# Kernel tuning notes

Hardware: AMD Instinct MI355X
Metric: run time of the kernel (lower is better)

The kernel has to match this reference:

```python
import jax, jax.numpy as jnp
import numpy as np

B, S, D = 2, 2048, 1024
H, DK, DV = 16, 64, 64
DFF = 4096
EPS_RMS = 1e-6


def setup_inputs() -> dict:
    key = jax.random.key(0)
    ks = jax.random.split(key, 10)
    sc = 0.02
    return {
        "x": jax.random.normal(ks[0], (B, S, D), jnp.float32),
        "w_q": jax.random.normal(ks[1], (D, H * DK), jnp.float32) * sc,
        "w_k": jax.random.normal(ks[2], (D, H * DK), jnp.float32) * sc,
        "w_v": jax.random.normal(ks[3], (D, H * DV), jnp.float32) * sc,
        "w_o": jax.random.normal(ks[4], (H * DV, D), jnp.float32) * sc,
        "w_gate": jax.random.normal(ks[5], (D, DFF), jnp.float32) * sc,
        "w_up": jax.random.normal(ks[6], (D, DFF), jnp.float32) * sc,
        "w_down": jax.random.normal(ks[7], (DFF, D), jnp.float32) * sc,
        "g1": jnp.ones((D,), jnp.float32),
        "g2": jnp.ones((D,), jnp.float32),
    }


def _rmsnorm(x, g):
    var = jnp.mean(jnp.square(x), axis=-1, keepdims=True)
    return x * jax.lax.rsqrt(var + EPS_RMS) * g


def _stable_softmax(s):
    # Faithful to source: exp(x) / (sum exp(x) + 1e-9); fully-masked rows -> 0.
    e = jnp.exp(s)
    return e / (jnp.sum(e, axis=-1, keepdims=True) + 1e-9)


def reference(x, w_q, w_k, w_v, w_o, w_gate, w_up, w_down, g1, g2):
    b, s, d = x.shape
    h = _rmsnorm(x, g1)
    q = (h @ w_q).reshape(b, s, H, DK).transpose(0, 2, 1, 3)  # [B,H,S,DK]
    k = (h @ w_k).reshape(b, s, H, DK).transpose(0, 2, 1, 3)
    v = (h @ w_v).reshape(b, s, H, DV).transpose(0, 2, 1, 3)
    scores = jnp.einsum("bhqd,bhkd->bhqk", q, k) / jnp.sqrt(jnp.asarray(DK, x.dtype))
    # triu with diagonal=0: self and future positions are masked
    mask = jnp.triu(jnp.ones((s, s), bool))
    scores = jnp.where(mask, -jnp.inf, scores)
    attn = _stable_softmax(scores)  # [B,H,S,S]
    av = jnp.einsum("bhqk,bhkd->bhqd", attn, v)
    av = av.transpose(0, 2, 1, 3).reshape(b, s, H * DV)
    x = x + av @ w_o  # residual 1
    h2 = _rmsnorm(x, g2)
    hidden = jax.nn.silu(h2 @ w_gate) * (h2 @ w_up)
    return x + hidden @ w_down  # residual 2
```

## Files before the change

kernel.cpp:

```cpp
#include <hip/hip_runtime.h>
#include <cstdint>
#include <cstddef>

typedef unsigned short u16;
typedef unsigned char u8;
typedef unsigned int u32;
typedef __bf16 bf16x8 __attribute__((ext_vector_type(8)));
typedef float floatx4 __attribute__((ext_vector_type(4)));
typedef float floatx16 __attribute__((ext_vector_type(16)));
typedef int i32x8 __attribute__((ext_vector_type(8)));

#define B_ 2
#define S_ 2048
#define D_ 1024
#define H_ 16
#define DFF_ 4096
#define BS_ 4096

__device__ __forceinline__ u16 f2bf(float f) {
  u32 u = __builtin_bit_cast(u32, f);
  u += 0x7fffu + ((u >> 16) & 1u);
  return (u16)(u >> 16);
}
__device__ __forceinline__ float bf2f(u16 h) {
  u32 u = ((u32)h) << 16;
  return __builtin_bit_cast(float, u);
}

__device__ __forceinline__ u32 f2e4m3(float f) {
  u32 u = __builtin_bit_cast(u32, f);
  const u32 s = (u >> 24) & 0x80u;
  const u32 au = u & 0x7fffffffu;
  if (au < 0x3c800000u) return s;
  if (au > 0x43e00000u) return s | 0x7eu;
  const u32 lsb = (au >> 20) & 1u;
  const u32 r = au + 0x0007ffffu + lsb;
  const u32 e = (r >> 23) & 0xffu;
  const u32 m = (r >> 20) & 7u;
  return s | (((e - 120u) & 0xfu) << 3) | m;
}

__device__ __forceinline__ void gl_lds16(const void* g, void* l) {
  __builtin_amdgcn_global_load_lds(
      (const __attribute__((address_space(1))) void*)g,
      (__attribute__((address_space(3))) void*)l, 16, 0, 0);
}

__global__ void prep_weights(const float* __restrict__ wq, const float* __restrict__ wk,
                             const float* __restrict__ wv, const float* __restrict__ wo,
                             const float* __restrict__ wg, const float* __restrict__ wu,
                             const float* __restrict__ wd,
                             u16* __restrict__ wqkv_t, u16* __restrict__ wo_t,
                             u8* __restrict__ wguf8, u16* __restrict__ wdn_t) {
  __shared__ float tile[32][33];
  const int id = blockIdx.x;
  const float* src;
  u16* dst = nullptr;
  int R, C, bx, by, mode;
  if (id < 3072) {
    const int which = id >> 10, lo = id & 1023;
    src = which == 0 ? wq : (which == 1 ? wk : wv);
    dst = wqkv_t + which * 1024 * 1024;
    R = 1024; C = 1024; bx = lo & 31; by = lo >> 5; mode = 0;
  } else if (id < 4096) {
    const int lo = id - 3072;
    src = wo; dst = wo_t; R = 1024; C = 1024; bx = lo & 31; by = lo >> 5; mode = 0;
  } else if (id < 8192) {
    const int lo = id - 4096;
    src = wg; R = 1024; C = 4096; bx = lo & 127; by = lo >> 7; mode = 1;
  } else if (id < 12288) {
    const int lo = id - 8192;
    src = wu; R = 1024; C = 4096; bx = lo & 127; by = lo >> 7; mode = 2;
  } else {
    const int lo = id - 12288;
    src = wd; dst = wdn_t; R = 4096; C = 1024; bx = lo & 31; by = lo >> 5; mode = 0;
  }
  const int tx = threadIdx.x, ty = threadIdx.y;
  const int c0 = bx * 32, r0 = by * 32;
#pragma unroll
  for (int i = 0; i < 4; i++)
    tile[ty + i * 8][tx] = src[(size_t)(r0 + ty + i * 8) * C + c0 + tx];
  __syncthreads();
  const int sx = ty * 32 + tx;
  const int oci = sx >> 3, cg = (sx & 7) * 4;
  const int oc = c0 + oci;
  const float v0 = tile[cg][oci], v1 = tile[cg + 1][oci];
  const float v2 = tile[cg + 2][oci], v3 = tile[cg + 3][oci];
  if (mode == 0) {
    uint2 o;
    o.x = (u32)f2bf(v0) | ((u32)f2bf(v1) << 16);
    o.y = (u32)f2bf(v2) | ((u32)f2bf(v3) << 16);
    *(uint2*)(dst + (size_t)oc * R + r0 + cg) = o;
  } else {
    const int orow = (oc >> 5) * 64 + (oc & 31) + (mode == 2 ? 32 : 0);
    const u32 p = f2e4m3(v0 * 64.f) | (f2e4m3(v1 * 64.f) << 8) |
                  (f2e4m3(v2 * 64.f) << 16) | (f2e4m3(v3 * 64.f) << 24);
    *(u32*)(wguf8 + (size_t)orow * 1024 + r0 + cg) = p;
  }
}

template <int F8>
__global__ __launch_bounds__(256) void rmsnorm_kernel(const float* __restrict__ x,
                                                      const float* __restrict__ g,
                                                      void* __restrict__ out) {
  const int row = blockIdx.x, t = threadIdx.x;
  const float4 v = ((const float4*)(x + (size_t)row * 1024))[t];
  float ss = v.x * v.x + v.y * v.y + v.z * v.z + v.w * v.w;
#pragma unroll
  for (int off = 32; off > 0; off >>= 1) ss += __shfl_xor(ss, off);
  __shared__ float red[4];
  if ((t & 63) == 0) red[t >> 6] = ss;
  __syncthreads();
  ss = red[0] + red[1] + red[2] + red[3];
  const float inv = rsqrtf(ss * (1.0f / 1024.0f) + 1e-6f);
  const float4 gv = ((const float4*)g)[t];
  const float y0 = v.x * inv * gv.x, y1 = v.y * inv * gv.y;
  const float y2 = v.z * inv * gv.z, y3 = v.w * inv * gv.w;
  if (F8) {
    const u32 p = f2e4m3(y0) | (f2e4m3(y1) << 8) | (f2e4m3(y2) << 16) | (f2e4m3(y3) << 24);
    ((u32*)out)[(size_t)row * 256 + t] = p;
  } else {
    uint2 o;
    o.x = (u32)f2bf(y0) | ((u32)f2bf(y1) << 16);
    o.y = (u32)f2bf(y2) | ((u32)f2bf(y3) << 16);
    ((uint2*)out)[(size_t)row * 256 + t] = o;
  }
}

template <int BN, int EPI>
__global__ __launch_bounds__(256) void gemm_bt(const u16* __restrict__ A,
                                               const u16* __restrict__ Bt,
                                               void* __restrict__ Cout,
                                               const float* __restrict__ res,
                                               u16* __restrict__ vTout,
                                               int M, int N, int K) {
  __shared__ u16 As[128 * 64];
  __shared__ u16 Bs[BN * 64];
  constexpr int NTI = BN / 64;
  constexpr int NSEG = 16 + BN / 8;
  constexpr int SPW = NSEG / 4;
  const int t = threadIdx.x, w = t >> 6, l = t & 63;
  const int m0 = blockIdx.y * 128, n0 = blockIdx.x * BN;
  const int wm = w >> 1, wn = w & 1;
  const int c31 = l & 31, khalf = l >> 5;

  const u16* gsrc[SPW];
  u16* ldst[SPW];
  {
    const int rl = l >> 3, ch = (l & 7) ^ rl;
#pragma unroll
    for (int i = 0; i < SPW; i++) {
      const int s = w * SPW + i;
      if (s < 16) {
        gsrc[i] = A + (size_t)(m0 + s * 8 + rl) * K + ch * 8;
        ldst[i] = As + s * 512;
      } else {
        gsrc[i] = Bt + (size_t)(n0 + (s - 16) * 8 + rl) * K + ch * 8;
        ldst[i] = Bs + (s - 16) * 512;
      }
    }
  }

  floatx16 acc[2][NTI] = {};

  for (int kk = 0; kk < K; kk += 64) {
    __syncthreads();
#pragma unroll
    for (int i = 0; i < SPW; i++) gl_lds16(gsrc[i], ldst[i]);
#pragma unroll
    for (int i = 0; i < SPW; i++) gsrc[i] += 64;
    __syncthreads();

#pragma unroll
    for (int ks = 0; ks < 4; ks++) {
      bf16x8 af[2], bfr[NTI];
#pragma unroll
      for (int mi = 0; mi < 2; mi++) {
        const int row = wm * 64 + mi * 32 + c31;
        const int e = (ks * 2 + khalf) ^ (row & 7);
        af[mi] = *(const bf16x8*)(As + row * 64 + e * 8);
      }
#pragma unroll
      for (int ni = 0; ni < NTI; ni++) {
        const int row = wn * (BN / 2) + ni * 32 + c31;
        const int e = (ks * 2 + khalf) ^ (row & 7);
        bfr[ni] = *(const bf16x8*)(Bs + row * 64 + e * 8);
      }
#pragma unroll
      for (int mi = 0; mi < 2; mi++)
#pragma unroll
        for (int ni = 0; ni < NTI; ni++)
          acc[mi][ni] = __builtin_amdgcn_mfma_f32_32x32x16_bf16(af[mi], bfr[ni],
                                                                acc[mi][ni], 0, 0, 0);
    }
  }

  if constexpr (EPI == 3) {
    if (n0 >= 2048) {
#pragma unroll
      for (int mi = 0; mi < 2; mi++)
#pragma unroll
        for (int ni = 0; ni < NTI; ni++) {
          const int col = n0 + wn * (BN / 2) + ni * 32 + c31 - 2048;
          const int hh = col >> 6, dv = col & 63;
          const int rbase = m0 + wm * 64 + mi * 32 + 4 * khalf;
          const int bb = rbase >> 11;
          u16* vp = vTout + (size_t)((bb * 16 + hh) * 64 + dv) * 2048 + (rbase & 2047);
#pragma unroll
          for (int rg = 0; rg < 4; rg++) {
            uint2 pk;
            pk.x = (u32)f2bf(acc[mi][ni][rg * 4 + 0]) |
                   ((u32)f2bf(acc[mi][ni][rg * 4 + 1]) << 16);
            pk.y = (u32)f2bf(acc[mi][ni][rg * 4 + 2]) |
                   ((u32)f2bf(acc[mi][ni][rg * 4 + 3]) << 16);
            *(uint2*)(vp + rg * 8) = pk;
          }
        }
      return;
    }
  }
#pragma unroll
  for (int mi = 0; mi < 2; mi++)
#pragma unroll
    for (int ni = 0; ni < NTI; ni++) {
      const int col = n0 + wn * (BN / 2) + ni * 32 + c31;
#pragma unroll
      for (int reg = 0; reg < 16; reg++) {
        const int row = m0 + wm * 64 + mi * 32 + (reg & 3) + 8 * (reg >> 2) + 4 * khalf;
        const size_t idx = (size_t)row * N + col;
        if (EPI == 1) ((float*)Cout)[idx] = acc[mi][ni][reg] + res[idx];
        else          ((u16*)Cout)[idx] = f2bf(acc[mi][ni][reg]);
      }
    }
}

__global__ __launch_bounds__(256) void gemm_f8(const u8* __restrict__ A,
                                               const u8* __restrict__ B,
                                               u16* __restrict__ hid,
                                               int M, int K) {
  __shared__ u8 As[128 * 64];
  __shared__ u8 Bs[128 * 64];
  const int t = threadIdx.x, w = t >> 6, l = t & 63;
  const int m0 = blockIdx.y * 128, n0 = blockIdx.x * 128;
  const int wm = w >> 1, wn = w & 1;
  const int c31 = l & 31, hf = l >> 5;

  const u8* gsrc[4];
  u8* ldst[4];
  {
    const int rl = l >> 2, ch = (l & 3) ^ ((l >> 3) & 3);
#pragma unroll
    for (int i = 0; i < 4; i++) {
      const int s = w * 4 + i;
      if (s < 8) {
        gsrc[i] = A + (size_t)(m0 + s * 16 + rl) * K + ch * 16;
        ldst[i] = As + s * 1024;
      } else {
        gsrc[i] = B + (size_t)(n0 + (s - 8) * 16 + rl) * K + ch * 16;
        ldst[i] = Bs + (s - 8) * 1024;
      }
    }
  }

  floatx16 acc[2][2] = {};

  for (int kk = 0; kk < K; kk += 64) {
    __syncthreads();
#pragma unroll
    for (int i = 0; i < 4; i++) gl_lds16(gsrc[i] + kk, ldst[i]);
    __syncthreads();

    i32x8 af[2], bf[2];
#pragma unroll
    for (int mi = 0; mi < 2; mi++) {
      const int r = wm * 64 + mi * 32 + c31;
      const int g = (r >> 1) & 3;
      const uint4 lo = *(const uint4*)(As + r * 64 + ((2 * hf) ^ g) * 16);
      const uint4 hi = *(const uint4*)(As + r * 64 + ((2 * hf + 1) ^ g) * 16);
      af[mi] = i32x8{(int)lo.x, (int)lo.y, (int)lo.z, (int)lo.w,
                     (int)hi.x, (int)hi.y, (int)hi.z, (int)hi.w};
    }
#pragma unroll
    for (int ni = 0; ni < 2; ni++) {
      const int r = wn * 64 + ni * 32 + c31;
      const int g = (r >> 1) & 3;
      const uint4 lo = *(const uint4*)(Bs + r * 64 + ((2 * hf) ^ g) * 16);
      const uint4 hi = *(const uint4*)(Bs + r * 64 + ((2 * hf + 1) ^ g) * 16);
      bf[ni] = i32x8{(int)lo.x, (int)lo.y, (int)lo.z, (int)lo.w,
                     (int)hi.x, (int)hi.y, (int)hi.z, (int)hi.w};
    }
#pragma unroll
    for (int mi = 0; mi < 2; mi++)
#pragma unroll
      for (int ni = 0; ni < 2; ni++)
        acc[mi][ni] = __builtin_amdgcn_mfma_scale_f32_32x32x64_f8f6f4(
            af[mi], bf[ni], acc[mi][ni], 0, 0,
            0, 0x7F7F7F7F,
            0, 0x79797979);
  }

#pragma unroll
  for (int mi = 0; mi < 2; mi++) {
    const int colo = ((int)blockIdx.x * 2 + wn) * 32 + c31;
#pragma unroll
    for (int reg = 0; reg < 16; reg++) {
      const int row = m0 + wm * 64 + mi * 32 + (reg & 3) + 8 * (reg >> 2) + 4 * hf;
      const float g = acc[mi][0][reg];
      const float u = acc[mi][1][reg];
      hid[(size_t)row * 4096 + colo] = f2bf(g / (1.f + __expf(-g)) * u);
    }
  }
}

__global__ __launch_bounds__(256) void attn_kernel(const u16* __restrict__ qkv,
                                                   const u16* __restrict__ vT,
                                                   u16* __restrict__ av) {
  __shared__ u16 SM[2 * 8192];
  __shared__ u16 Ps[4 * 2048];
  const int t = threadIdx.x, w = t >> 6, l = t & 63;
  const int lrow = l & 15, lk = l >> 4;
  const int bh = blockIdx.x;
  const int b = bh >> 4, h = bh & 15;
  const int qt = 15 - (int)blockIdx.y;
  const int qbase = qt * 128 + w * 32;
  const int ktmax = 2 * qt + 1;
  u16* Pw = Ps + w * 2048;

  bf16x8 aq[2][2];
#pragma unroll
  for (int sub = 0; sub < 2; sub++)
#pragma unroll
    for (int half = 0; half < 2; half++)
      aq[sub][half] = *(const bf16x8*)(qkv + (size_t)(b * S_ + qbase + sub * 16 + lrow) * 3072 +
                                       h * 64 + half * 32 + lk * 8);

  const u16* gcur[4];
  int gstep[4], loff[4];
#pragma unroll
  for (int i = 0; i < 4; i++) {
    const int c = w + 4 * i;
    const int half = (c >> 2) & 1, grp = c & 3;
    if (c < 8) {
      gcur[i] = qkv + (size_t)(b * S_ + grp * 16 + (l >> 2)) * 3072 + D_ + h * 64 +
                half * 32 + (l & 3) * 8;
      gstep[i] = 64 * 3072;
      loff[i] = half * 2048 + grp * 512;
    } else {
      gcur[i] = vT + (size_t)(bh * 64 + grp * 16 + (l >> 2)) * S_ + half * 32 + (l & 3) * 8;
      gstep[i] = 64;
      loff[i] = 4096 + half * 2048 + grp * 512;
    }
  }

  floatx4 oacc[2][4] = {};
  float den[2] = {0.f, 0.f};

  int cur = 0;
#pragma unroll
  for (int i = 0; i < 4; i++) { gl_lds16(gcur[i], SM + loff[i]); gcur[i] += gstep[i]; }

  for (int kt = 0; kt <= ktmax; kt++) {
    __syncthreads();
    if (kt < ktmax) {
#pragma unroll
      for (int i = 0; i < 4; i++) {
        gl_lds16(gcur[i], SM + (cur ^ 1) * 8192 + loff[i]);
        gcur[i] += gstep[i];
      }
    }
    const u16* Kbuf = SM + cur * 8192;
    const u16* Vbuf = Kbuf + 4096;

    bf16x8 bk[4][2];
#pragma unroll
    for (int ct = 0; ct < 4; ct++)
#pragma unroll
      for (int half = 0; half < 2; half++)
        bk[ct][half] = *(const bf16x8*)(Kbuf + half * 2048 + (ct * 16 + lrow) * 32 + lk * 8);

    floatx4 sf[2][4] = {};
#pragma unroll
    for (int sub = 0; sub < 2; sub++)
#pragma unroll
      for (int ct = 0; ct < 4; ct++) {
        sf[sub][ct] = __builtin_amdgcn_mfma_f32_16x16x32_bf16(bk[ct][0], aq[sub][0],
                                                              sf[sub][ct], 0, 0, 0);
        sf[sub][ct] = __builtin_amdgcn_mfma_f32_16x16x32_bf16(bk[ct][1], aq[sub][1],
                                                              sf[sub][ct], 0, 0, 0);
      }

#pragma unroll
    for (int sub = 0; sub < 2; sub++) {
      const int qp = qbase + sub * 16 + lrow;
      const int prow = sub * 16 + lrow;
#pragma unroll
      for (int ct = 0; ct < 4; ct++) {
        const int kb = kt * 64 + ct * 16 + lk * 4;
        float p0 = (kb + 0 < qp) ? __expf(sf[sub][ct][0] * 0.125f) : 0.f;
        float p1 = (kb + 1 < qp) ? __expf(sf[sub][ct][1] * 0.125f) : 0.f;
        float p2 = (kb + 2 < qp) ? __expf(sf[sub][ct][2] * 0.125f) : 0.f;
        float p3 = (kb + 3 < qp) ? __expf(sf[sub][ct][3] * 0.125f) : 0.f;
        den[sub] += (p0 + p1) + (p2 + p3);
        uint2 pk;
        pk.x = (u32)f2bf(p0) | ((u32)f2bf(p1) << 16);
        pk.y = (u32)f2bf(p2) | ((u32)f2bf(p3) << 16);
        *(uint2*)(Pw + prow * 64 + (((2 * ct + (lk >> 1)) ^ (lrow & 7)) << 3) +
                  (lk & 1) * 4) = pk;
      }
    }

    bf16x8 ap[2][2], bv[4][2];
#pragma unroll
    for (int sub = 0; sub < 2; sub++)
#pragma unroll
      for (int kh = 0; kh < 2; kh++) {
        const int prow = sub * 16 + lrow;
        ap[sub][kh] = *(const bf16x8*)(Pw + prow * 64 + (((kh * 4 + lk) ^ (prow & 7)) << 3));
      }
#pragma unroll
    for (int ni = 0; ni < 4; ni++)
#pragma unroll
      for (int kh = 0; kh < 2; kh++)
        bv[ni][kh] = *(const bf16x8*)(Vbuf + kh * 2048 + (ni * 16 + lrow) * 32 + lk * 8);
#pragma unroll
    for (int sub = 0; sub < 2; sub++)
#pragma unroll
      for (int ni = 0; ni < 4; ni++) {
        oacc[sub][ni] = __builtin_amdgcn_mfma_f32_16x16x32_bf16(ap[sub][0], bv[ni][0],
                                                                oacc[sub][ni], 0, 0, 0);
        oacc[sub][ni] = __builtin_amdgcn_mfma_f32_16x16x32_bf16(ap[sub][1], bv[ni][1],
                                                                oacc[sub][ni], 0, 0, 0);
      }
    cur ^= 1;
  }

#pragma unroll
  for (int sub = 0; sub < 2; sub++) {
    den[sub] += __shfl_xor(den[sub], 16);
    den[sub] += __shfl_xor(den[sub], 32);
  }
  float dq[2][4];
#pragma unroll
  for (int sub = 0; sub < 2; sub++)
#pragma unroll
    for (int r = 0; r < 4; r++)
      dq[sub][r] = __shfl(den[sub], lk * 4 + r);

#pragma unroll
  for (int sub = 0; sub < 2; sub++)
#pragma unroll
    for (int ni = 0; ni < 4; ni++)
#pragma unroll
      for (int r = 0; r < 4; r++) {
        const int row = qbase + sub * 16 + lk * 4 + r;
        const int col = h * 64 + ni * 16 + lrow;
        av[(size_t)(b * S_ + row) * 1024 + col] = f2bf(oacc[sub][ni][r] / (dq[sub][r] + 1e-9f));
      }
}

#define OFF_WQKV 0u
#define OFF_WO   6291456u
#define OFF_WGU8 8388608u
#define OFF_WDN  16777216u
#define OFF_H1   25165824u
#define OFF_QKV  33554432u
#define OFF_VT   58720256u
#define OFF_AV   67108864u
#define OFF_X1   75497472u
#define OFF_H2F8 92274688u
#define OFF_HID  96468992u

extern "C" void kernel_launch(void* const* d_in, const int* in_sizes, int n_in,
                              void* d_out, int out_size, void* d_ws, size_t ws_size,
                              hipStream_t stream) {
  const float* x      = (const float*)d_in[0];
  const float* w_q    = (const float*)d_in[1];
  const float* w_k    = (const float*)d_in[2];
  const float* w_v    = (const float*)d_in[3];
  const float* w_o    = (const float*)d_in[4];
  const float* w_gate = (const float*)d_in[5];
  const float* w_up   = (const float*)d_in[6];
  const float* w_down = (const float*)d_in[7];
  const float* g1     = (const float*)d_in[8];
  const float* g2     = (const float*)d_in[9];

  char* ws = (char*)d_ws;
  u16* wqkv_t = (u16*)(ws + OFF_WQKV);
  u16* wo_t   = (u16*)(ws + OFF_WO);
  u8*  wguf8  = (u8*)(ws + OFF_WGU8);
  u16* wdn_t  = (u16*)(ws + OFF_WDN);
  u16* h1     = (u16*)(ws + OFF_H1);
  u16* qkv    = (u16*)(ws + OFF_QKV);
  u16* vT     = (u16*)(ws + OFF_VT);
  u16* av     = (u16*)(ws + OFF_AV);
  float* x1   = (float*)(ws + OFF_X1);
  u8*  h2f8   = (u8*)(ws + OFF_H2F8);
  u16* hid    = (u16*)(ws + OFF_HID);
  float* out  = (float*)d_out;

  prep_weights<<<16384, dim3(32, 8), 0, stream>>>(w_q, w_k, w_v, w_o, w_gate, w_up, w_down,
                                                  wqkv_t, wo_t, wguf8, wdn_t);

  rmsnorm_kernel<0><<<BS_, 256, 0, stream>>>(x, g1, h1);
  gemm_bt<128, 3><<<dim3(3072 / 128, BS_ / 128), 256, 0, stream>>>(
      h1, wqkv_t, qkv, nullptr, vT, BS_, 3072, 1024);
  attn_kernel<<<dim3(32, 16), 256, 0, stream>>>(qkv, vT, av);
  gemm_bt<64, 1><<<dim3(1024 / 64, BS_ / 128), 256, 0, stream>>>(
      av, wo_t, x1, x, nullptr, BS_, 1024, 1024);
  rmsnorm_kernel<1><<<BS_, 256, 0, stream>>>(x1, g2, h2f8);
  gemm_f8<<<dim3(4096 / 64, BS_ / 128), 256, 0, stream>>>(h2f8, wguf8, hid, BS_, 1024);
  gemm_bt<64, 1><<<dim3(1024 / 64, BS_ / 128), 256, 0, stream>>>(
      hid, wdn_t, out, x1, nullptr, BS_, 1024, 4096);
}
```

Baseline: 346.4 us.

## Double-buffer LDS loads in BN=64 GEMMs and add XCD-aware block swizzle

Adds a two-stage LDS pipeline to the bf16 GEMM used for the output projection and the down projection. The next K-tile's global-to-LDS load is issued before the MFMA work on the current tile, so load latency overlaps compute and one barrier per step is dropped. All GEMMs also remap block indices so consecutive tiles land on the same XCD, aiming for better L2 reuse. The cost is doubled LDS for the pipelined variant and the extra remap arithmetic.

```diff
diff --git a/kernel.cpp b/kernel.cpp
--- a/kernel.cpp
+++ b/kernel.cpp
@@ -44,6 +44,14 @@
   __builtin_amdgcn_global_load_lds(
       (const __attribute__((address_space(1))) void*)g,
       (__attribute__((address_space(3))) void*)l, 16, 0, 0);
+}
+
+__device__ __forceinline__ void xcd_swz(int GX, int GY, int& bx, int& by) {
+  int flat = by * GX + bx;
+  const int q = (GX * GY) >> 3;
+  flat = (flat & 7) * q + (flat >> 3);
+  bx = flat % GX;
+  by = flat / GX;
 }
 
 __global__ void prep_weights(const float* __restrict__ wq, const float* __restrict__ wk,
@@ -127,25 +135,59 @@
   }
 }
 
-template <int BN, int EPI>
+template <int BN>
+__device__ __forceinline__ void bt_step(const u16* Asb, const u16* Bsb,
+                                        floatx16 (&acc)[2][BN / 64],
+                                        int wm, int wn, int c31, int khalf) {
+  constexpr int NTI = BN / 64;
+#pragma unroll
+  for (int ks = 0; ks < 4; ks++) {
+    bf16x8 af[2], bfr[NTI];
+#pragma unroll
+    for (int mi = 0; mi < 2; mi++) {
+      const int row = wm * 64 + mi * 32 + c31;
+      const int e = (ks * 2 + khalf) ^ (row & 7);
+      af[mi] = *(const bf16x8*)(Asb + row * 64 + e * 8);
+    }
+#pragma unroll
+    for (int ni = 0; ni < NTI; ni++) {
+      const int row = wn * (BN / 2) + ni * 32 + c31;
+      const int e = (ks * 2 + khalf) ^ (row & 7);
+      bfr[ni] = *(const bf16x8*)(Bsb + row * 64 + e * 8);
+    }
+#pragma unroll
+    for (int mi = 0; mi < 2; mi++)
+#pragma unroll
+      for (int ni = 0; ni < NTI; ni++)
+        acc[mi][ni] = __builtin_amdgcn_mfma_f32_32x32x16_bf16(af[mi], bfr[ni],
+                                                              acc[mi][ni], 0, 0, 0);
+  }
+}
+
+template <int BN, int EPI, int PIPE>
 __global__ __launch_bounds__(256) void gemm_bt(const u16* __restrict__ A,
                                                const u16* __restrict__ Bt,
                                                void* __restrict__ Cout,
                                                const float* __restrict__ res,
                                                u16* __restrict__ vTout,
                                                int M, int N, int K) {
-  __shared__ u16 As[128 * 64];
-  __shared__ u16 Bs[BN * 64];
+  constexpr int NBUF = PIPE ? 2 : 1;
+  __shared__ u16 As[NBUF][128 * 64];
+  __shared__ u16 Bs[NBUF][BN * 64];
   constexpr int NTI = BN / 64;
   constexpr int NSEG = 16 + BN / 8;
   constexpr int SPW = NSEG / 4;
   const int t = threadIdx.x, w = t >> 6, l = t & 63;
-  const int m0 = blockIdx.y * 128, n0 = blockIdx.x * BN;
+
+  int bx = (int)blockIdx.x, by = (int)blockIdx.y;
+  xcd_swz((int)gridDim.x, (int)gridDim.y, bx, by);
+  const int m0 = by * 128, n0 = bx * BN;
   const int wm = w >> 1, wn = w & 1;
   const int c31 = l & 31, khalf = l >> 5;
 
   const u16* gsrc[SPW];
-  u16* ldst[SPW];
+  u16* ld0[SPW];
+  u16* ld1[SPW];
   {
     const int rl = l >> 3, ch = (l & 7) ^ rl;
 #pragma unroll
@@ -153,45 +195,52 @@
       const int s = w * SPW + i;
       if (s < 16) {
         gsrc[i] = A + (size_t)(m0 + s * 8 + rl) * K + ch * 8;
-        ldst[i] = As + s * 512;
+        ld0[i] = As[0] + s * 512;
+        ld1[i] = As[NBUF - 1] + s * 512;
       } else {
         gsrc[i] = Bt + (size_t)(n0 + (s - 16) * 8 + rl) * K + ch * 8;
-        ldst[i] = Bs + (s - 16) * 512;
+        ld0[i] = Bs[0] + (s - 16) * 512;
+        ld1[i] = Bs[NBUF - 1] + (s - 16) * 512;
       }
     }
   }
 
   floatx16 acc[2][NTI] = {};
 
-  for (int kk = 0; kk < K; kk += 64) {
-    __syncthreads();
-#pragma unroll
-    for (int i = 0; i < SPW; i++) gl_lds16(gsrc[i], ldst[i]);
+  if constexpr (!PIPE) {
+    for (int kk = 0; kk < K; kk += 64) {
+      __syncthreads();
+#pragma unroll
+      for (int i = 0; i < SPW; i++) gl_lds16(gsrc[i], ld0[i]);
+#pragma unroll
+      for (int i = 0; i < SPW; i++) gsrc[i] += 64;
+      __syncthreads();
+      bt_step<BN>(As[0], Bs[0], acc, wm, wn, c31, khalf);
+    }
+  } else {
+#pragma unroll
+    for (int i = 0; i < SPW; i++) gl_lds16(gsrc[i], ld0[i]);
 #pragma unroll
     for (int i = 0; i < SPW; i++) gsrc[i] += 64;
-    __syncthreads();
-
-#pragma unroll
-    for (int ks = 0; ks < 4; ks++) {
-      bf16x8 af[2], bfr[NTI];
-#pragma unroll
-      for (int mi = 0; mi < 2; mi++) {
-        const int row = wm * 64 + mi * 32 + c31;
-        const int e = (ks * 2 + khalf) ^ (row & 7);
-        af[mi] = *(const bf16x8*)(As + row * 64 + e * 8);
-      }
-#pragma unroll
-      for (int ni = 0; ni < NTI; ni++) {
-        const int row = wn * (BN / 2) + ni * 32 + c31;
-        const int e = (ks * 2 + khalf) ^ (row & 7);
-        bfr[ni] = *(const bf16x8*)(Bs + row * 64 + e * 8);
-      }
-#pragma unroll
-      for (int mi = 0; mi < 2; mi++)
-#pragma unroll
-        for (int ni = 0; ni < NTI; ni++)
-          acc[mi][ni] = __builtin_amdgcn_mfma_f32_32x32x16_bf16(af[mi], bfr[ni],
-                                                                acc[mi][ni], 0, 0, 0);
+    asm volatile("s_waitcnt vmcnt(0)" ::: "memory");
+    __builtin_amdgcn_s_barrier();
+    for (int kk = 0; kk < K; kk += 128) {
+#pragma unroll
+      for (int i = 0; i < SPW; i++) gl_lds16(gsrc[i], ld1[i]);
+#pragma unroll
+      for (int i = 0; i < SPW; i++) gsrc[i] += 64;
+      bt_step<BN>(As[0], Bs[0], acc, wm, wn, c31, khalf);
+      asm volatile("s_waitcnt vmcnt(0)" ::: "memory");
+      __builtin_amdgcn_s_barrier();
+      if (kk + 128 < K) {
+#pragma unroll
+        for (int i = 0; i < SPW; i++) gl_lds16(gsrc[i], ld0[i]);
+#pragma unroll
+        for (int i = 0; i < SPW; i++) gsrc[i] += 64;
+      }
+      bt_step<BN>(As[NBUF - 1], Bs[NBUF - 1], acc, wm, wn, c31, khalf);
+      asm volatile("s_waitcnt vmcnt(0)" ::: "memory");
+      __builtin_amdgcn_s_barrier();
     }
   }
 
@@ -241,7 +290,9 @@
   __shared__ u8 As[128 * 64];
   __shared__ u8 Bs[128 * 64];
   const int t = threadIdx.x, w = t >> 6, l = t & 63;
-  const int m0 = blockIdx.y * 128, n0 = blockIdx.x * 128;
+  int bx = (int)blockIdx.x, by = (int)blockIdx.y;
+  xcd_swz((int)gridDim.x, (int)gridDim.y, bx, by);
+  const int m0 = by * 128, n0 = bx * 128;
   const int wm = w >> 1, wn = w & 1;
   const int c31 = l & 31, hf = l >> 5;
 
@@ -301,7 +352,7 @@
 
 #pragma unroll
   for (int mi = 0; mi < 2; mi++) {
-    const int colo = ((int)blockIdx.x * 2 + wn) * 32 + c31;
+    const int colo = (bx * 2 + wn) * 32 + c31;
 #pragma unroll
     for (int reg = 0; reg < 16; reg++) {
       const int row = m0 + wm * 64 + mi * 32 + (reg & 3) + 8 * (reg >> 2) + 4 * hf;
@@ -502,13 +553,13 @@
                                                   wqkv_t, wo_t, wguf8, wdn_t);
 
   rmsnorm_kernel<0><<<BS_, 256, 0, stream>>>(x, g1, h1);
-  gemm_bt<128, 3><<<dim3(3072 / 128, BS_ / 128), 256, 0, stream>>>(
+  gemm_bt<128, 3, 0><<<dim3(3072 / 128, BS_ / 128), 256, 0, stream>>>(
       h1, wqkv_t, qkv, nullptr, vT, BS_, 3072, 1024);
   attn_kernel<<<dim3(32, 16), 256, 0, stream>>>(qkv, vT, av);
-  gemm_bt<64, 1><<<dim3(1024 / 64, BS_ / 128), 256, 0, stream>>>(
+  gemm_bt<64, 1, 1><<<dim3(1024 / 64, BS_ / 128), 256, 0, stream>>>(
       av, wo_t, x1, x, nullptr, BS_, 1024, 1024);
   rmsnorm_kernel<1><<<BS_, 256, 0, stream>>>(x1, g2, h2f8);
   gemm_f8<<<dim3(4096 / 64, BS_ / 128), 256, 0, stream>>>(h2f8, wguf8, hid, BS_, 1024);
-  gemm_bt<64, 1><<<dim3(1024 / 64, BS_ / 128), 256, 0, stream>>>(
+  gemm_bt<64, 1, 1><<<dim3(1024 / 64, BS_ / 128), 256, 0, stream>>>(
       hid, wdn_t, out, x1, nullptr, BS_, 1024, 4096);
 }
```

Measured after the change: 342.2 us. No clear change (-1.2%).
